# Kernel optimization log

Hardware: AMD Instinct MI355X
Metric: run time of the kernel (lower is better)

Reference implementation:

```python
import jax, jax.numpy as jnp
import numpy as np

EPS = 1e-5

def _ln(x, g, b):
    m = jnp.mean(x, -1, keepdims=True)
    v = jnp.mean((x - m) ** 2, -1, keepdims=True)
    return (x - m) * jax.lax.rsqrt(v + EPS) * g + b

def _lstm(x, Wih, Whh, bih, bhh):
    # x: [B, T, D]; torch gate order i, f, g, o; h0 = c0 = 0
    B = x.shape[0]
    H = Whh.shape[1]
    h0 = jnp.zeros((B, H), x.dtype)
    c0 = jnp.zeros((B, H), x.dtype)
    bias = bih + bhh
    def step(carry, xt):
        h, c = carry
        gates = xt @ Wih.T + h @ Whh.T + bias  # [B, 4H]
        i, f, g, o = jnp.split(gates, 4, axis=-1)
        c = jax.nn.sigmoid(f) * c + jax.nn.sigmoid(i) * jnp.tanh(g)
        h = jax.nn.sigmoid(o) * jnp.tanh(c)
        return (h, c), h
    _, hs = jax.lax.scan(step, (h0, c0), jnp.swapaxes(x, 0, 1))
    return jnp.swapaxes(hs, 0, 1)  # [B, T, H]

def setup_inputs() -> dict:
    key = jax.random.key(0)
    ks = jax.random.split(key, 20)
    N, C, F, T = 4, 64, 256, 256
    D, H = 128, 32  # LSTM in/out
    s = 0.05
    inp = {
        "inputs": jax.random.normal(ks[0], (N, C, F, T, 2), jnp.float32),
        "ln1_g": jnp.ones((D,), jnp.float32), "ln1_b": jnp.zeros((D,), jnp.float32),
        "Wih_q": s * jax.random.normal(ks[1], (4 * H, D), jnp.float32),
        "Whh_q": s * jax.random.normal(ks[2], (4 * H, H), jnp.float32),
        "bih_q": s * jax.random.normal(ks[3], (4 * H,), jnp.float32),
        "bhh_q": s * jax.random.normal(ks[4], (4 * H,), jnp.float32),
        "Wih_k": s * jax.random.normal(ks[5], (4 * H, D), jnp.float32),
        "Whh_k": s * jax.random.normal(ks[6], (4 * H, H), jnp.float32),
        "bih_k": s * jax.random.normal(ks[7], (4 * H,), jnp.float32),
        "bhh_k": s * jax.random.normal(ks[8], (4 * H,), jnp.float32),
        "Wih_v": s * jax.random.normal(ks[9], (4 * H, D), jnp.float32),
        "Whh_v": s * jax.random.normal(ks[10], (4 * H, H), jnp.float32),
        "bih_v": s * jax.random.normal(ks[11], (4 * H,), jnp.float32),
        "bhh_v": s * jax.random.normal(ks[12], (4 * H,), jnp.float32),
        "ln2_g": jnp.ones((H,), jnp.float32), "ln2_b": jnp.zeros((H,), jnp.float32),
        "Wr": s * jax.random.normal(ks[13], (C, H // 2), jnp.float32),
        "br": s * jax.random.normal(ks[14], (C,), jnp.float32),
        "Wi": s * jax.random.normal(ks[15], (C, H // 2), jnp.float32),
        "bi": s * jax.random.normal(ks[16], (C,), jnp.float32),
        "ln3_g": jnp.ones((C,), jnp.float32), "ln3_b": jnp.zeros((C,), jnp.float32),
        "prelu_a": jnp.full((1,), 0.25, jnp.float32),
    }
    return inp

def reference(inputs, ln1_g, ln1_b,
              Wih_q, Whh_q, bih_q, bhh_q,
              Wih_k, Whh_k, bih_k, bhh_k,
              Wih_v, Whh_v, bih_v, bhh_v,
              ln2_g, ln2_b, Wr, br, Wi, bi,
              ln3_g, ln3_b, prelu_a):
    N, C, F, T, ri = inputs.shape
    # [N,C,F,T,2] -> [N*F, T, C, 2] -> concat real/imag -> [N*F, T, 2C]
    x4 = jnp.transpose(inputs, (0, 2, 3, 1, 4)).reshape(N * F, T, C, ri)
    x = jnp.concatenate([x4[..., 0], x4[..., 1]], axis=-1)  # [B, T, 128]
    # Self_Attention_T_RICAT (single head)
    xn = _ln(x, ln1_g, ln1_b)
    q = _lstm(xn, Wih_q, Whh_q, bih_q, bhh_q)  # [B, T, 32]
    k = _lstm(xn, Wih_k, Whh_k, bih_k, bhh_k)
    v = _lstm(xn, Wih_v, Whh_v, bih_v, bhh_v)
    energy = jnp.einsum('btf,bsf->bts', q, k) / 4.0  # / 16**0.5
    mask = jnp.tril(jnp.ones((T, T), x.dtype))
    attn = jax.nn.softmax(energy * mask, axis=-1)  # multiplicative mask, as in source
    wv = jnp.einsum('bts,bsf->btf', attn, v)  # [B, T, 32]
    out = _ln(wv, ln2_g, ln2_b)
    # complex-valued linear fusion
    xr, xi = jnp.split(out, 2, axis=-1)  # [B, T, 16] each
    lr_r = xr @ Wr.T + br
    li_i = xi @ Wi.T + bi
    lr_i = xi @ Wr.T + br
    li_r = xr @ Wi.T + bi
    out_real = (lr_r - li_i).reshape(N, F, T, C).transpose(0, 3, 1, 2)  # [N,C,F,T]
    out_imag = (lr_i + li_r).reshape(N, F, T, C).transpose(0, 3, 1, 2)
    outs = jnp.stack([out_real, out_imag], axis=-1)  # [N,C,F,T,2]
    outs_t = jnp.swapaxes(outs, 1, 4)  # [N,2,F,T,C]
    outs = jnp.swapaxes(_ln(outs_t, ln3_g, ln3_b), 1, 4)
    outs = jnp.where(outs >= 0, outs, prelu_a[0] * outs)  # PReLU (eval mode, dropout=identity)
    return outs + inputs
```

## Files before the change

kernel.cpp:

```cpp
#include <hip/hip_runtime.h>
#include <hip/hip_bf16.h>
#include <stddef.h>


typedef __bf16 bf16x8 __attribute__((ext_vector_type(8)));
typedef float f32x4 __attribute__((ext_vector_type(4)));

__device__ __forceinline__ ushort f2bf(float x) {
    uint u = __builtin_bit_cast(uint, x);
    uint r = (u + 0x7fffu + ((u >> 16) & 1u)) >> 16;
    return (ushort)r;
}

__device__ __forceinline__ float fsig(float x) {
    return __builtin_amdgcn_rcpf(1.f + __expf(-x));
}
__device__ __forceinline__ float ftanh(float x) {
    return 1.f - 2.f * __builtin_amdgcn_rcpf(__expf(2.f * x) + 1.f);
}
__device__ __forceinline__ float wredsum(float v) {
#pragma unroll
    for (int off = 32; off; off >>= 1) v += __shfl_xor(v, off);
    return v;
}
__device__ __forceinline__ float hredsum(float v) {
#pragma unroll
    for (int off = 16; off; off >>= 1) v += __shfl_xor(v, off);
    return v;
}

__global__ __launch_bounds__(256) void k_prep(const float* __restrict__ in,
                                              const float* __restrict__ g1,
                                              const float* __restrict__ b1,
                                              ushort* __restrict__ xn) {
    __shared__ float xl[32][129];
    const int n = blockIdx.z, f = blockIdx.y, t0 = blockIdx.x * 32;
    const int tid = threadIdx.x;
    const int c = tid >> 2, q = tid & 3;
    const float* src = in + ((size_t)(n * 64 + c) * 256 + f) * 512 + t0 * 2 + q * 16;
#pragma unroll
    for (int e = 0; e < 4; ++e) {
        float4 v4 = *(const float4*)(src + e * 4);
        int dt = q * 8 + e * 2;
        xl[dt][c]          = v4.x;
        xl[dt][c + 64]     = v4.y;
        xl[dt + 1][c]      = v4.z;
        xl[dt + 1][c + 64] = v4.w;
    }
    __syncthreads();
    const int lane = tid & 63, w = tid >> 6;
    const int b = n * 256 + f;
#pragma unroll 1
    for (int r = 0; r < 8; ++r) {
        int dt = w * 8 + r;
        float a = xl[dt][lane], bb = xl[dt][lane + 64];
        float s = wredsum(a + bb);
        float mean = s * 0.0078125f;
        float da = a - mean, db = bb - mean;
        float var = wredsum(da * da + db * db) * 0.0078125f;
        float inv = __builtin_amdgcn_rsqf(var + 1e-5f);
        size_t base = ((size_t)b * 256 + (t0 + dt)) * 128;
        xn[base + lane]      = f2bf(da * inv * g1[lane] + b1[lane]);
        xn[base + lane + 64] = f2bf(db * inv * g1[lane + 64] + b1[lane + 64]);
    }
}

__global__ __launch_bounds__(256) void k_gemm(const ushort* __restrict__ xn,
                                              const float* __restrict__ Wq,
                                              const float* __restrict__ Wk,
                                              const float* __restrict__ Wv,
                                              const float* __restrict__ bihq, const float* __restrict__ bhhq,
                                              const float* __restrict__ bihk, const float* __restrict__ bhhk,
                                              const float* __restrict__ bihv, const float* __restrict__ bhhv,
                                              ushort* __restrict__ gx) {
    __shared__ ushort a_lds[128 * 136];
    __shared__ ushort w_lds[128 * 136];
    const int tid = threadIdx.x;
    const int m0 = blockIdx.x * 128;

#pragma unroll
    for (int p = 0; p < 8; ++p) {
        int idx = p * 256 + tid;
        int r = idx >> 4, c = idx & 15;
        *(uint4*)&a_lds[r * 136 + c * 8] =
            *(const uint4*)(xn + (size_t)(m0 + r) * 128 + c * 8);
    }

    const int w = tid >> 6, lane = tid & 63;
    const int wr = w >> 1, wc = w & 1;
    const int row16 = lane & 15, koct = lane >> 4;

#pragma unroll 1
    for (int l = 0; l < 3; ++l) {
        const float* W   = (l == 0) ? Wq   : (l == 1) ? Wk   : Wv;
        const float* bih = (l == 0) ? bihq : (l == 1) ? bihk : bihv;
        const float* bhh = (l == 0) ? bhhq : (l == 1) ? bhhk : bhhv;
        __syncthreads();
#pragma unroll
        for (int p = 0; p < 8; ++p) {
            int idx = p * 256 + tid;
            int r = idx >> 4, c = idx & 15;
            const float* wp = W + (size_t)r * 128 + c * 8;
            float4 wa = *(const float4*)wp;
            float4 wb = *(const float4*)(wp + 4);
            union { ushort u[8]; uint4 v; } pk;
            pk.u[0] = f2bf(wa.x); pk.u[1] = f2bf(wa.y); pk.u[2] = f2bf(wa.z); pk.u[3] = f2bf(wa.w);
            pk.u[4] = f2bf(wb.x); pk.u[5] = f2bf(wb.y); pk.u[6] = f2bf(wb.z); pk.u[7] = f2bf(wb.w);
            *(uint4*)&w_lds[r * 136 + c * 8] = pk.v;
        }
        __syncthreads();

        f32x4 acc[4][4];
#pragma unroll
        for (int mi = 0; mi < 4; ++mi)
#pragma unroll
            for (int ni = 0; ni < 4; ++ni) acc[mi][ni] = (f32x4){0.f, 0.f, 0.f, 0.f};

#pragma unroll
        for (int ki = 0; ki < 4; ++ki) {
            bf16x8 af[4], bfr[4];
#pragma unroll
            for (int mi = 0; mi < 4; ++mi)
                af[mi] = *(const bf16x8*)&a_lds[(wr * 64 + mi * 16 + row16) * 136 + ki * 32 + koct * 8];
#pragma unroll
            for (int ni = 0; ni < 4; ++ni)
                bfr[ni] = *(const bf16x8*)&w_lds[(wc * 64 + ni * 16 + row16) * 136 + ki * 32 + koct * 8];
#pragma unroll
            for (int mi = 0; mi < 4; ++mi)
#pragma unroll
                for (int ni = 0; ni < 4; ++ni)
                    acc[mi][ni] = __builtin_amdgcn_mfma_f32_16x16x32_bf16(af[mi], bfr[ni], acc[mi][ni], 0, 0, 0);
        }

#pragma unroll
        for (int ni = 0; ni < 4; ++ni) {
            int g = wc * 64 + ni * 16 + row16;
            float bsv = bih[g] + bhh[g];
            int j = g & 31, gi = g >> 5;
            int s = j * 4 + gi;
#pragma unroll
            for (int mi = 0; mi < 4; ++mi)
#pragma unroll
                for (int q = 0; q < 4; ++q) {
                    size_t m = (size_t)m0 + wr * 64 + mi * 16 + koct * 4 + q;
                    gx[m * 384 + l * 128 + s] = f2bf(acc[mi][ni][q] + bsv);
                }
        }
    }
}

__global__ __launch_bounds__(128, 1) void k_lstm(const ushort* __restrict__ gx,
                                                 const float* __restrict__ Whq,
                                                 const float* __restrict__ Whk,
                                                 const float* __restrict__ Whv,
                                                 ushort* __restrict__ qkv) {
    __shared__ ushort H[2][16][40];
    const int tid = threadIdx.x;
    const int w = tid >> 6, lane = tid & 63;
    const int r16 = lane & 15, koct = lane >> 4;
    const int l = blockIdx.x >> 6, bgrp = blockIdx.x & 63;
    const int b = bgrp * 16 + r16;
    const float* Wh = (l == 0) ? Whq : (l == 1) ? Whk : Whv;

    bf16x8 wf[4];
#pragma unroll
    for (int gg = 0; gg < 4; ++gg) {
        int g = 4 * w + gg;
        int jA = 8 * (r16 >> 2) + g;
        int giA = r16 & 3;
        const float* wp = Wh + (size_t)(giA * 32 + jA) * 32 + koct * 8;
        float4 wa = *(const float4*)wp;
        float4 wb = *(const float4*)(wp + 4);
        union { ushort u[8]; bf16x8 v; } pk;
        pk.u[0] = f2bf(wa.x); pk.u[1] = f2bf(wa.y); pk.u[2] = f2bf(wa.z); pk.u[3] = f2bf(wa.w);
        pk.u[4] = f2bf(wb.x); pk.u[5] = f2bf(wb.y); pk.u[6] = f2bf(wb.z); pk.u[7] = f2bf(wb.w);
        wf[gg] = pk.v;
    }

    const ushort* gp = gx + (size_t)b * 98304 + l * 128 + koct * 32 + w * 16;
    uint4 pf[4][2];
#pragma unroll
    for (int tt = 0; tt < 4; ++tt) {
        pf[tt][0] = *(const uint4*)(gp + (size_t)tt * 384);
        pf[tt][1] = *(const uint4*)(gp + (size_t)tt * 384 + 8);
    }

    if (tid < 64) {
        ((uint*)&H[0][0][0])[tid];
    }
    for (int i = tid; i < 320; i += 128) ((uint*)&H[0][0][0])[i] = 0;
    __syncthreads();

    float cst[4] = {0.f, 0.f, 0.f, 0.f};
    ushort* outp = qkv + ((size_t)(l * 1024 + b)) * 8192 + koct * 8 + w * 4;

#pragma unroll 4
    for (int t = 0; t < 256; ++t) {
        const int sl = t & 3;
        const int p = t & 1;
        bf16x8 hf = *(const bf16x8*)&H[p][r16][koct * 8];

        uint u[8];
        u[0] = pf[sl][0].x; u[1] = pf[sl][0].y; u[2] = pf[sl][0].z; u[3] = pf[sl][0].w;
        u[4] = pf[sl][1].x; u[5] = pf[sl][1].y; u[6] = pf[sl][1].z; u[7] = pf[sl][1].w;
        pf[sl][0] = *(const uint4*)(gp + (size_t)(t + 4) * 384);
        pf[sl][1] = *(const uint4*)(gp + (size_t)(t + 4) * 384 + 8);

        f32x4 acc[4];
#pragma unroll
        for (int gg = 0; gg < 4; ++gg)
#pragma unroll
            for (int q = 0; q < 4; ++q) {
                int v = gg * 4 + q;
                uint w32 = u[v >> 1];
                acc[gg][q] = __builtin_bit_cast(float, (v & 1) ? (w32 & 0xffff0000u) : (w32 << 16));
            }
#pragma unroll
        for (int gg = 0; gg < 4; ++gg)
            acc[gg] = __builtin_amdgcn_mfma_f32_16x16x32_bf16(wf[gg], hf, acc[gg], 0, 0, 0);

        float hv[4];
#pragma unroll
        for (int gg = 0; gg < 4; ++gg) {
            float gi = acc[gg][0], gf = acc[gg][1], gg2 = acc[gg][2], go = acc[gg][3];
            float cN = fsig(gf) * cst[gg] + fsig(gi) * ftanh(gg2);
            cst[gg] = cN;
            hv[gg] = fsig(go) * ftanh(cN);
        }
        uint2 hp;
        __asm__ volatile("v_cvt_pk_bf16_f32 %0, %1, %2" : "=v"(hp.x) : "v"(hv[0]), "v"(hv[1]));
        __asm__ volatile("v_cvt_pk_bf16_f32 %0, %1, %2" : "=v"(hp.y) : "v"(hv[2]), "v"(hv[3]));
        *(uint2*)&H[p ^ 1][r16][koct * 8 + w * 4] = hp;
        *(uint2*)(outp + (size_t)t * 32) = hp;
        __syncthreads();
    }
}

__global__ __launch_bounds__(256) void k_attn(const ushort* __restrict__ qkvb,
                                              float* __restrict__ wvout) {
    __shared__ ushort k_sw[256 * 32];
    __shared__ ushort vt_sw[32 * 256];
    __shared__ ushort p_sw[4][16 * 256];
    const int tid = threadIdx.x, w = tid >> 6, lane = tid & 63;
    const int b = blockIdx.x;
    const ushort* qb = qkvb + (size_t)b * 8192;
    const ushort* kb = qkvb + 8388608 + (size_t)b * 8192;
    const ushort* vb = qkvb + 16777216 + (size_t)b * 8192;
#pragma unroll
    for (int p = 0; p < 4; ++p) {
        int idx = p * 256 + tid;
        int s = idx >> 2, cc = idx & 3;
        uint4 kv = *(const uint4*)(kb + s * 32 + cc * 8);
        int cK = cc ^ ((s >> 1) & 3);
        *(uint4*)&k_sw[s * 32 + cK * 8] = kv;
        uint4 vv = *(const uint4*)(vb + s * 32 + cc * 8);
        union { uint4 v; ushort u[8]; } un; un.v = vv;
#pragma unroll
        for (int e = 0; e < 8; ++e) {
            int row = cc * 8 + e;
            vt_sw[row * 256 + (((s >> 3) ^ (row & 7)) << 3) + (s & 7)] = un.u[e];
        }
    }
    __syncthreads();
    const int r16 = lane & 15, koct = lane >> 4;
    ushort* pw = p_sw[w];
    bf16x8 qf[4];
#pragma unroll
    for (int i = 0; i < 4; ++i) {
        int t = (w * 4 + i) * 16 + r16;
        qf[i] = *(const bf16x8*)(qb + t * 32 + koct * 8);
    }
#pragma unroll 1
    for (int i = 0; i < 4; ++i) {
        const int tb = (w * 4 + i) * 16;
        f32x4 acc[16];
#pragma unroll
        for (int st = 0; st < 16; ++st) acc[st] = (f32x4){0.f, 0.f, 0.f, 0.f};
#pragma unroll
        for (int st = 0; st < 16; ++st) {
            int s = st * 16 + r16;
            int cK = koct ^ ((s >> 1) & 3);
            bf16x8 kf = *(const bf16x8*)&k_sw[s * 32 + cK * 8];
            acc[st] = __builtin_amdgcn_mfma_f32_16x16x32_bf16(qf[i], kf, acc[st], 0, 0, 0);
        }
        float mx[4] = {-1e30f, -1e30f, -1e30f, -1e30f};
#pragma unroll
        for (int st = 0; st < 16; ++st) {
            int s = st * 16 + r16;
#pragma unroll
            for (int q = 0; q < 4; ++q) {
                int t = tb + koct * 4 + q;
                float v = (s <= t) ? acc[st][q] * 0.25f : 0.f;
                acc[st][q] = v;
                mx[q] = fmaxf(mx[q], v);
            }
        }
#pragma unroll
        for (int off = 1; off < 16; off <<= 1)
#pragma unroll
            for (int q = 0; q < 4; ++q) mx[q] = fmaxf(mx[q], __shfl_xor(mx[q], off));
        float sm[4] = {0.f, 0.f, 0.f, 0.f};
#pragma unroll
        for (int st = 0; st < 16; ++st)
#pragma unroll
            for (int q = 0; q < 4; ++q) {
                float p = __expf(acc[st][q] - mx[q]);
                acc[st][q] = p; sm[q] += p;
            }
#pragma unroll
        for (int off = 1; off < 16; off <<= 1)
#pragma unroll
            for (int q = 0; q < 4; ++q) sm[q] += __shfl_xor(sm[q], off);
        float rs[4];
#pragma unroll
        for (int q = 0; q < 4; ++q) rs[q] = __builtin_amdgcn_rcpf(sm[q]);
#pragma unroll
        for (int st = 0; st < 16; ++st) {
            int schunk = st * 2 + (r16 >> 3), sl = r16 & 7;
#pragma unroll
            for (int q = 0; q < 4; ++q) {
                int tl = koct * 4 + q;
                pw[tl * 256 + ((schunk ^ (tl & 7)) << 3) + sl] = f2bf(acc[st][q] * rs[q]);
            }
        }
        __asm__ volatile("s_waitcnt lgkmcnt(0)" ::: "memory");
        f32x4 oa[2];
        oa[0] = (f32x4){0.f, 0.f, 0.f, 0.f};
        oa[1] = (f32x4){0.f, 0.f, 0.f, 0.f};
#pragma unroll
        for (int ks = 0; ks < 8; ++ks) {
            int kc = ks * 4 + koct;
            bf16x8 pa = *(const bf16x8*)&pw[r16 * 256 + ((kc ^ (r16 & 7)) << 3)];
#pragma unroll
            for (int n = 0; n < 2; ++n) {
                int row = n * 16 + r16;
                bf16x8 vf = *(const bf16x8*)&vt_sw[row * 256 + ((kc ^ (row & 7)) << 3)];
                oa[n] = __builtin_amdgcn_mfma_f32_16x16x32_bf16(pa, vf, oa[n], 0, 0, 0);
            }
        }
#pragma unroll
        for (int n = 0; n < 2; ++n)
#pragma unroll
            for (int q = 0; q < 4; ++q)
                wvout[((size_t)b * 256 + tb + koct * 4 + q) * 32 + n * 16 + r16] = oa[n][q];
    }
}

__global__ __launch_bounds__(256) void k_post(const float* __restrict__ wv,
                                              const float* __restrict__ in,
                                              const float* __restrict__ g2,
                                              const float* __restrict__ b2,
                                              const float* __restrict__ Wr,
                                              const float* __restrict__ br,
                                              const float* __restrict__ Wi,
                                              const float* __restrict__ bi,
                                              const float* __restrict__ g3,
                                              const float* __restrict__ b3,
                                              const float* __restrict__ pa,
                                              float* __restrict__ outp) {
    __shared__ float xv[32][33];
    __shared__ float wr_l[64][17], wi_l[64][17];
    __shared__ float out_s[64][65];
    const int tid = threadIdx.x;
    const int n = blockIdx.z, f = blockIdx.y, t0 = blockIdx.x * 32;
    const int b = n * 256 + f;
    for (int idx = tid; idx < 1024; idx += 256) {
        int dt = idx >> 5, j = idx & 31;
        xv[dt][j] = wv[((size_t)b * 256 + t0 + dt) * 32 + j];
        int cc = idx >> 4, jjj = idx & 15;
        wr_l[cc][jjj] = Wr[idx];
        wi_l[cc][jjj] = Wi[idx];
    }
    __syncthreads();
    const int lane = tid & 63, w = tid >> 6;
#pragma unroll 1
    for (int r = 0; r < 4; ++r) {
        int dt = w * 8 + r * 2 + (lane >> 5);
        int j = lane & 31;
        float v = xv[dt][j];
        float mean = hredsum(v) * 0.03125f;
        float d = v - mean;
        float var = hredsum(d * d) * 0.03125f;
        float inv = __builtin_amdgcn_rsqf(var + 1e-5f);
        xv[dt][j] = d * inv * g2[j] + b2[j];
    }
    __syncthreads();
    const int c = lane;
    const float g3c = g3[c], b3c = b3[c];
    const float bd = br[c] - bi[c], bsum = br[c] + bi[c];
    const float alpha = pa[0];
#pragma unroll 1
    for (int r = 0; r < 8; ++r) {
        int dt = w * 8 + r;
        float re = 0.f, im = 0.f;
#pragma unroll
        for (int j = 0; j < 16; ++j) {
            float xr = xv[dt][j], xi2 = xv[dt][16 + j];
            float wrv = wr_l[c][j], wiv = wi_l[c][j];
            re += xr * wrv; re -= xi2 * wiv;
            im += xi2 * wrv; im += xr * wiv;
        }
        re += bd; im += bsum;
        float mR = wredsum(re) * 0.015625f;
        float dR = re - mR;
        float vR = wredsum(dR * dR) * 0.015625f;
        float nR = dR * __builtin_amdgcn_rsqf(vR + 1e-5f) * g3c + b3c;
        nR = (nR >= 0.f) ? nR : alpha * nR;
        float mI = wredsum(im) * 0.015625f;
        float dI = im - mI;
        float vI = wredsum(dI * dI) * 0.015625f;
        float nI = dI * __builtin_amdgcn_rsqf(vI + 1e-5f) * g3c + b3c;
        nI = (nI >= 0.f) ? nI : alpha * nI;
        out_s[c][dt * 2]     = nR;
        out_s[c][dt * 2 + 1] = nI;
    }
    __syncthreads();
    const int cc = tid >> 2, q = tid & 3;
    size_t base = ((size_t)(n * 64 + cc) * 256 + f) * 512 + t0 * 2 + q * 16;
#pragma unroll
    for (int e = 0; e < 4; ++e) {
        float4 iv = *(const float4*)(in + base + e * 4);
        int k0 = q * 16 + e * 4;
        float4 ov;
        ov.x = out_s[cc][k0]     + iv.x;
        ov.y = out_s[cc][k0 + 1] + iv.y;
        ov.z = out_s[cc][k0 + 2] + iv.z;
        ov.w = out_s[cc][k0 + 3] + iv.w;
        *(float4*)(outp + base + e * 4) = ov;
    }
}

extern "C" void kernel_launch(void* const* d_in, const int* in_sizes, int n_in,
                              void* d_out, int out_size, void* d_ws, size_t ws_size,
                              hipStream_t stream) {
    const float* in   = (const float*)d_in[0];
    const float* g1   = (const float*)d_in[1];
    const float* b1   = (const float*)d_in[2];
    const float* Wq   = (const float*)d_in[3];
    const float* Whq  = (const float*)d_in[4];
    const float* bihq = (const float*)d_in[5];
    const float* bhhq = (const float*)d_in[6];
    const float* Wk   = (const float*)d_in[7];
    const float* Whk  = (const float*)d_in[8];
    const float* bihk = (const float*)d_in[9];
    const float* bhhk = (const float*)d_in[10];
    const float* Wv   = (const float*)d_in[11];
    const float* Whv  = (const float*)d_in[12];
    const float* bihv = (const float*)d_in[13];
    const float* bhhv = (const float*)d_in[14];
    const float* g2   = (const float*)d_in[15];
    const float* b2   = (const float*)d_in[16];
    const float* Wr   = (const float*)d_in[17];
    const float* br   = (const float*)d_in[18];
    const float* Wi   = (const float*)d_in[19];
    const float* bi   = (const float*)d_in[20];
    const float* g3   = (const float*)d_in[21];
    const float* b3   = (const float*)d_in[22];
    const float* pa   = (const float*)d_in[23];
    float* outp = (float*)d_out;

    ushort* gxb  = (ushort*)d_ws;
    ushort* xnb  = (ushort*)((char*)d_ws + 201326592);
    ushort* qkvb = (ushort*)((char*)d_ws + 268435456);
    float*  wvb  = (float*)((char*)d_ws + 318767104);

    k_prep<<<dim3(8, 256, 4), dim3(256), 0, stream>>>(in, g1, b1, xnb);
    k_gemm<<<dim3(2048), dim3(256), 0, stream>>>(xnb, Wq, Wk, Wv,
                                                 bihq, bhhq, bihk, bhhk, bihv, bhhv, gxb);
    k_lstm<<<dim3(192), dim3(128), 0, stream>>>(gxb, Whq, Whk, Whv, qkvb);
    k_attn<<<dim3(1024), dim3(256), 0, stream>>>(qkvb, wvb);
    k_post<<<dim3(8, 256, 4), dim3(256), 0, stream>>>(wvb, in, g2, b2,
                                                      Wr, br, Wi, bi, g3, b3, pa, outp);
}
```

Before: 513.8 us.

## Use bf16 MFMA for complex linear projection in post kernel

Replaces the scalar per-channel complex linear (16-wide dot products per time step, with full wave reductions for LayerNorm) in k_post with a single 16x16x32 bf16 MFMA per channel tile. Sign and Wr/Wi selection are folded into the packed weight fragments, and LayerNorm statistics are computed in one pass from sum and sum-of-squares using 16-lane shuffles. Weights now come straight from global memory into registers instead of shared memory. This lowers precision to bf16 for the projection and uses single-pass variance, which adds rounding error. It also drops a dead shared-memory read in the LSTM kernel.

```diff
diff --git a/kernel.cpp b/kernel.cpp
--- a/kernel.cpp
+++ b/kernel.cpp
@@ -185,9 +185,6 @@
         pf[tt][1] = *(const uint4*)(gp + (size_t)tt * 384 + 8);
     }
 
-    if (tid < 64) {
-        ((uint*)&H[0][0][0])[tid];
-    }
     for (int i = tid; i < 320; i += 128) ((uint*)&H[0][0][0])[i] = 0;
     __syncthreads();
 
@@ -358,21 +355,44 @@
                                               const float* __restrict__ b3,
                                               const float* __restrict__ pa,
                                               float* __restrict__ outp) {
-    __shared__ float xv[32][33];
-    __shared__ float wr_l[64][17], wi_l[64][17];
+    __shared__ float xv[32][36];
     __shared__ float out_s[64][65];
     const int tid = threadIdx.x;
     const int n = blockIdx.z, f = blockIdx.y, t0 = blockIdx.x * 32;
     const int b = n * 256 + f;
+    const int lane = tid & 63, w = tid >> 6;
+    const int r16 = lane & 15, koct = lane >> 4;
+    const int tt = w & 1, ri = w >> 1;
+
     for (int idx = tid; idx < 1024; idx += 256) {
         int dt = idx >> 5, j = idx & 31;
         xv[dt][j] = wv[((size_t)b * 256 + t0 + dt) * 32 + j];
-        int cc = idx >> 4, jjj = idx & 15;
-        wr_l[cc][jjj] = Wr[idx];
-        wi_l[cc][jjj] = Wi[idx];
-    }
+    }
+
+    bf16x8 bfr[4];
+    float bias_v[4], g3v[4], b3v[4];
+    const int kofs = (koct < 2) ? koct * 8 : (koct - 2) * 8;
+#pragma unroll
+    for (int ct = 0; ct < 4; ++ct) {
+        int c = ct * 16 + r16;
+        const float* srcW = (ri == 0) ? ((koct < 2) ? Wr : Wi)
+                                      : ((koct < 2) ? Wi : Wr);
+        float sgn = (ri == 0 && koct >= 2) ? -1.f : 1.f;
+        float4 wa = *(const float4*)(srcW + c * 16 + kofs);
+        float4 wb = *(const float4*)(srcW + c * 16 + kofs + 4);
+        union { ushort u[8]; bf16x8 v; } pk;
+        pk.u[0] = f2bf(sgn * wa.x); pk.u[1] = f2bf(sgn * wa.y);
+        pk.u[2] = f2bf(sgn * wa.z); pk.u[3] = f2bf(sgn * wa.w);
+        pk.u[4] = f2bf(sgn * wb.x); pk.u[5] = f2bf(sgn * wb.y);
+        pk.u[6] = f2bf(sgn * wb.z); pk.u[7] = f2bf(sgn * wb.w);
+        bfr[ct] = pk.v;
+        bias_v[ct] = (ri == 0) ? (br[c] - bi[c]) : (br[c] + bi[c]);
+        g3v[ct] = g3[c];
+        b3v[ct] = b3[c];
+    }
+    const float alpha = pa[0];
     __syncthreads();
-    const int lane = tid & 63, w = tid >> 6;
+
 #pragma unroll 1
     for (int r = 0; r < 4; ++r) {
         int dt = w * 8 + r * 2 + (lane >> 5);
@@ -385,36 +405,57 @@
         xv[dt][j] = d * inv * g2[j] + b2[j];
     }
     __syncthreads();
-    const int c = lane;
-    const float g3c = g3[c], b3c = b3[c];
-    const float bd = br[c] - bi[c], bsum = br[c] + bi[c];
-    const float alpha = pa[0];
-#pragma unroll 1
-    for (int r = 0; r < 8; ++r) {
-        int dt = w * 8 + r;
-        float re = 0.f, im = 0.f;
-#pragma unroll
-        for (int j = 0; j < 16; ++j) {
-            float xr = xv[dt][j], xi2 = xv[dt][16 + j];
-            float wrv = wr_l[c][j], wiv = wi_l[c][j];
-            re += xr * wrv; re -= xi2 * wiv;
-            im += xi2 * wrv; im += xr * wiv;
-        }
-        re += bd; im += bsum;
-        float mR = wredsum(re) * 0.015625f;
-        float dR = re - mR;
-        float vR = wredsum(dR * dR) * 0.015625f;
-        float nR = dR * __builtin_amdgcn_rsqf(vR + 1e-5f) * g3c + b3c;
-        nR = (nR >= 0.f) ? nR : alpha * nR;
-        float mI = wredsum(im) * 0.015625f;
-        float dI = im - mI;
-        float vI = wredsum(dI * dI) * 0.015625f;
-        float nI = dI * __builtin_amdgcn_rsqf(vI + 1e-5f) * g3c + b3c;
-        nI = (nI >= 0.f) ? nI : alpha * nI;
-        out_s[c][dt * 2]     = nR;
-        out_s[c][dt * 2 + 1] = nI;
+
+    const float* xrow = &xv[tt * 16 + r16][koct * 8];
+    float4 a0 = *(const float4*)xrow;
+    float4 a1 = *(const float4*)(xrow + 4);
+    uint4 ap;
+    __asm__ volatile("v_cvt_pk_bf16_f32 %0, %1, %2" : "=v"(ap.x) : "v"(a0.x), "v"(a0.y));
+    __asm__ volatile("v_cvt_pk_bf16_f32 %0, %1, %2" : "=v"(ap.y) : "v"(a0.z), "v"(a0.w));
+    __asm__ volatile("v_cvt_pk_bf16_f32 %0, %1, %2" : "=v"(ap.z) : "v"(a1.x), "v"(a1.y));
+    __asm__ volatile("v_cvt_pk_bf16_f32 %0, %1, %2" : "=v"(ap.w) : "v"(a1.z), "v"(a1.w));
+    bf16x8 af = __builtin_bit_cast(bf16x8, ap);
+
+    f32x4 acc[4];
+#pragma unroll
+    for (int ct = 0; ct < 4; ++ct) {
+        acc[ct] = (f32x4){0.f, 0.f, 0.f, 0.f};
+        acc[ct] = __builtin_amdgcn_mfma_f32_16x16x32_bf16(af, bfr[ct], acc[ct], 0, 0, 0);
+    }
+
+    float val[4][4];
+    float s[4] = {0.f, 0.f, 0.f, 0.f}, sq[4] = {0.f, 0.f, 0.f, 0.f};
+#pragma unroll
+    for (int ct = 0; ct < 4; ++ct)
+#pragma unroll
+        for (int q = 0; q < 4; ++q) {
+            float v = acc[ct][q] + bias_v[ct];
+            val[ct][q] = v;
+            s[q] += v;
+            sq[q] += v * v;
+        }
+#pragma unroll
+    for (int off = 1; off < 16; off <<= 1)
+#pragma unroll
+        for (int q = 0; q < 4; ++q) {
+            s[q]  += __shfl_xor(s[q], off);
+            sq[q] += __shfl_xor(sq[q], off);
+        }
+#pragma unroll
+    for (int q = 0; q < 4; ++q) {
+        float m = s[q] * 0.015625f;
+        float var = fmaxf(sq[q] * 0.015625f - m * m, 0.f);
+        float inv = __builtin_amdgcn_rsqf(var + 1e-5f);
+        int t2 = (tt * 16 + koct * 4 + q) * 2 + ri;
+#pragma unroll
+        for (int ct = 0; ct < 4; ++ct) {
+            float nv = (val[ct][q] - m) * inv * g3v[ct] + b3v[ct];
+            nv = (nv >= 0.f) ? nv : alpha * nv;
+            out_s[ct * 16 + r16][t2] = nv;
+        }
     }
     __syncthreads();
+
     const int cc = tid >> 2, q = tid & 3;
     size_t base = ((size_t)(n * 64 + cc) * 256 + f) * 512 + t0 * 2 + q * 16;
 #pragma unroll
```

Measured after the change: 474.6 us. -7.6%, faster.
